# Kernel tuning notes

Hardware: AMD Instinct MI355X
Metric: run time of the kernel (lower is better)

## Reference

```python
import jax, jax.numpy as jnp
import numpy as np

EMB = 256
HID = 512
LAYERS = 4
VOCAB = 256
B = 16
T = 2048


def setup_inputs() -> dict:
    key = jax.random.key(0)
    ks = jax.random.split(key, 2 * LAYERS + 4)
    x = jax.random.randint(ks[0], (B, T), 0, VOCAB)
    emb = jax.random.uniform(ks[1], (VOCAB, EMB), minval=-0.1, maxval=0.1, dtype=jnp.float32)
    out = {"x": x, "emb": emb}
    for i in range(LAYERS):
        din = EMB if i == 0 else HID
        W = jax.random.normal(ks[2 + 2 * i], (din, 3 * HID), dtype=jnp.float32) * (1.0 / np.sqrt(din)).astype(np.float32)
        b = jnp.zeros((3 * HID,), jnp.float32)
        out[f"W{i}"] = W
        out[f"b{i}"] = b
    out["decW"] = jax.random.uniform(ks[2 + 2 * LAYERS], (HID, VOCAB), minval=-0.1, maxval=0.1, dtype=jnp.float32)
    out["decb"] = jnp.zeros((VOCAB,), jnp.float32)
    return out


def _fo_pool(z, f):
    # c_t = f_t * c_{t-1} + (1 - f_t) * z_t, c_{-1} = 0; z,f: (T, B, H)
    def step(c, zf):
        zt, ft = zf
        c = ft * c + (1.0 - ft) * zt
        return c, c
    c0 = jnp.zeros(z.shape[1:], z.dtype)
    _, C = jax.lax.scan(step, c0, (z, f))
    return C


def _qrnn_layer(x, W, b):
    # x: (T, B, D) time-major. One Linear producing Z,F,O gates, fo-pool, output gate.
    Y = jnp.einsum('tbd,dh->tbh', x, W) + b
    z, f, o = jnp.split(Y, 3, axis=-1)
    C = _fo_pool(jnp.tanh(z), jax.nn.sigmoid(f))
    return jax.nn.sigmoid(o) * C


def _dilated_layer(x, rate, W, b):
    # Fold time into batch by dilation rate, run QRNN, unfold (matches DRNN._prepare_inputs/_split_outputs)
    Tn, Bn, D = x.shape
    pad = (-Tn) % rate
    if pad:
        x = jnp.concatenate([x, jnp.zeros((pad, Bn, D), x.dtype)], axis=0)
    Tr = x.shape[0] // rate
    # dilated[t, j*B + b] = x[t*rate + j, b]
    xd = x.reshape(Tr, rate, Bn, D).reshape(Tr, rate * Bn, D)
    yd = _qrnn_layer(xd, W, b)  # (Tr, rate*B, H)
    Hd = yd.shape[-1]
    y = yd.reshape(Tr, rate, Bn, Hd).reshape(Tr * rate, Bn, Hd)[:Tn]
    return y


def reference(x, emb, W0, b0, W1, b1, W2, b2, W3, b3, decW, decb):
    h = emb[x]                    # (B, T, EMB) embedding lookup (dropout is identity at eval)
    h = h.transpose(1, 0, 2)      # time-major (T, B, EMB)
    Ws = [W0, W1, W2, W3]
    bs = [b0, b1, b2, b3]
    for i in range(LAYERS):
        h = _dilated_layer(h, 2 ** i, Ws[i], bs[i])
    h = h.transpose(1, 0, 2)      # (B, T, HID)
    return jnp.einsum('bth,hv->btv', h, decW) + decb
```

## Files before the change

### kernel.cpp

```cpp
#include <hip/hip_runtime.h>

#define TSEQ 2048
#define BATCH 16
#define EMBD 256
#define HID 512
#define NG 1536
#define NVOCAB 256
#define MROWS (TSEQ*BATCH)
#define CM 8192

typedef __attribute__((ext_vector_type(8))) unsigned short u16x8;
typedef __attribute__((ext_vector_type(8))) short s16x8;
typedef __attribute__((ext_vector_type(4))) float f32x4;

__device__ __forceinline__ float bf2f(unsigned short u) {
  union { unsigned u; float f; } x; x.u = ((unsigned)u) << 16; return x.f;
}
__device__ __forceinline__ unsigned short f2bf(float v) {
  union { float f; unsigned u; } x; x.f = v;
  unsigned r = (x.u + 0x7fffu + ((x.u >> 16) & 1u)) >> 16;
  return (unsigned short)r;
}
__device__ __forceinline__ float fast_rcp(float x) { return __builtin_amdgcn_rcpf(x); }
__device__ __forceinline__ float fast_sigmoid(float x) {
  float e = __builtin_amdgcn_exp2f(fminf(-1.442695041f * x, 80.f));
  return fast_rcp(1.f + e);
}
__device__ __forceinline__ float fast_tanh(float x) {
  float e = __builtin_amdgcn_exp2f(fminf(-2.885390082f * x, 80.f));
  return (1.f - e) * fast_rcp(1.f + e);
}
__device__ __forceinline__ void lds_cp16(const void* g, void* l) {
  __builtin_amdgcn_global_load_lds((const __attribute__((address_space(1))) void*)g,
                                   (__attribute__((address_space(3))) void*)l, 16, 0, 0);
}

__global__ __launch_bounds__(256) void embed_k(const int* __restrict__ x,
                                               const float* __restrict__ emb,
                                               unsigned short* __restrict__ H0) {
  int idx = blockIdx.x * 256 + threadIdx.x;
  int m = idx >> 5, e8 = (idx & 31) * 8;
  int tok = x[(m & 15) * TSEQ + (m >> 4)];
  const float* e = emb + (size_t)tok * EMBD + e8;
  float4 v0 = *(const float4*)e;
  float4 v1 = *(const float4*)(e + 4);
  u16x8 o;
  o[0]=f2bf(v0.x); o[1]=f2bf(v0.y); o[2]=f2bf(v0.z); o[3]=f2bf(v0.w);
  o[4]=f2bf(v1.x); o[5]=f2bf(v1.y); o[6]=f2bf(v1.z); o[7]=f2bf(v1.w);
  *(u16x8*)(H0 + (size_t)m * EMBD + e8) = o;
}

__global__ __launch_bounds__(256) void wt_k(const float* __restrict__ W,
                                            unsigned short* __restrict__ Wt,
                                            int K, int N) {
  __shared__ float tile[32][33];
  int n0 = blockIdx.x * 32, k0 = blockIdx.y * 32;
  int tx = threadIdx.x, ty = threadIdx.y;
#pragma unroll
  for (int i = 0; i < 4; ++i)
    tile[ty + i * 8][tx] = W[(size_t)(k0 + ty + i * 8) * N + n0 + tx];
  __syncthreads();
#pragma unroll
  for (int i = 0; i < 4; ++i)
    Wt[(size_t)(n0 + ty + i * 8) * K + k0 + tx] = f2bf(tile[tx][ty + i * 8]);
}

template <int K, int EPI>
__global__ __launch_bounds__(256) void gemm_k(const unsigned short* __restrict__ A,
                                              const unsigned short* __restrict__ Bt,
                                              const float* __restrict__ bias,
                                              unsigned short* __restrict__ Yg,
                                              float* __restrict__ Out) {
  __shared__ unsigned short smem[16384];
  unsigned short* sA = smem;
  unsigned short* sB = smem + 4096;
  const int tid = threadIdx.x;
  const int m0 = blockIdx.y * 128;
  const int n0 = blockIdx.x * 128;
  const int lane = tid & 63, wave = tid >> 6;
  const int wm = (wave >> 1) * 64, wn = (wave & 1) * 64;
  const int l15 = lane & 15, lg = lane >> 4;

  f32x4 acc[4][4] = {};

  for (int k0 = 0; k0 < K; k0 += 32) {
#pragma unroll
    for (int j = 0; j < 2; ++j) {
      int fl = j * 256 + tid;
      int m = fl >> 2;
      int cl = ((fl & 3) << 4) ^ (((m >> 1) & 3) << 4);
      lds_cp16(A + (size_t)(m0 + m) * K + k0 + (cl >> 1), &sA[fl * 8]);
      lds_cp16(Bt + (size_t)(n0 + m) * K + k0 + (cl >> 1), &sB[fl * 8]);
    }
    __syncthreads();

    s16x8 af[4], bf[4];
#pragma unroll
    for (int i = 0; i < 4; ++i) {
      int ma = wm + i * 16 + l15;
      int ca = (lg * 16) ^ (((ma >> 1) & 3) << 4);
      af[i] = *(const s16x8*)&sA[ma * 32 + (ca >> 1)];
      int nb = wn + i * 16 + l15;
      int cb = (lg * 16) ^ (((nb >> 1) & 3) << 4);
      bf[i] = *(const s16x8*)&sB[nb * 32 + (cb >> 1)];
    }
#pragma unroll
    for (int i = 0; i < 4; ++i)
#pragma unroll
      for (int j = 0; j < 4; ++j)
        acc[i][j] = __builtin_amdgcn_mfma_f32_16x16x32_bf16(af[i], bf[j], acc[i][j], 0, 0, 0);
    __syncthreads();
  }

  if (EPI == 0) {
    const int acttype = n0 >> 9;
#pragma unroll
    for (int i = 0; i < 4; ++i)
#pragma unroll
      for (int j = 0; j < 4; ++j)
#pragma unroll
        for (int r = 0; r < 4; ++r) {
          int mm = wm + i * 16 + lg * 4 + r;
          int nn = wn + j * 16 + l15;
          float v = acc[i][j][r] + bias[n0 + nn];
          v = (acttype == 0) ? fast_tanh(v) : fast_sigmoid(v);
          smem[mm * 128 + (nn ^ ((mm & 7) << 3))] = f2bf(v);
        }
    __syncthreads();
#pragma unroll
    for (int it = 0; it < 8; ++it) {
      int fl = it * 256 + tid;
      int mm = fl >> 4, ng = (fl & 15) * 8;
      u16x8 v = *(const u16x8*)&smem[mm * 128 + (ng ^ ((mm & 7) << 3))];
      *(u16x8*)(Yg + (size_t)(m0 + mm) * NG + n0 + ng) = v;
    }
  } else {
#pragma unroll
    for (int i = 0; i < 4; ++i)
#pragma unroll
      for (int j = 0; j < 4; ++j)
#pragma unroll
        for (int r = 0; r < 4; ++r) {
          int mmg = m0 + wm + i * 16 + lg * 4 + r;
          int nn = n0 + wn + j * 16 + l15;
          float v = acc[i][j][r] + bias[nn];
          int b = mmg & 15, t = mmg >> 4;
          Out[((size_t)b * TSEQ + t) * NVOCAB + nn] = v;
        }
  }
}

template <int LGS>
__global__ __launch_bounds__(256) void scan2_k(const unsigned short* __restrict__ Y,
                                               unsigned short* __restrict__ Hout,
                                               float* __restrict__ cst,
                                               int m0, int init) {
  const int S = 1 << LGS;
  const int HS = 1 << LGS;
  const int NSEG = 1 << (8 - LGS);
  __shared__ float As[256], Bs[256], Ci[256];

  const int tid = threadIdx.x;
  const int hi = tid & (HS - 1), seg = tid >> LGS;
  const int hg = blockIdx.x & ((2 * NSEG) - 1);
  const int s = blockIdx.x >> (9 - LGS);
  const int h = hg * HS + hi;
  const int mb = seg * 32 * S + s;

  float a = 1.f, c = 0.f;
#pragma unroll 8
  for (int t = 0; t < 32; ++t) {
    size_t ro = (size_t)(mb + t * S) * NG;
    float z = bf2f(Y[ro + h]);
    float f = bf2f(Y[ro + 512 + h]);
    a *= f;
    c = __builtin_fmaf(f, c - z, z);
  }
  As[seg * HS + hi] = a;
  Bs[seg * HS + hi] = c;
  __syncthreads();

  if (seg == 0) {
    float cc = init ? 0.f : cst[s * 512 + h];
#pragma unroll
    for (int k = 0; k < NSEG; ++k) {
      Ci[k * HS + hi] = cc;
      cc = __builtin_fmaf(As[k * HS + hi], cc, Bs[k * HS + hi]);
    }
    cst[s * 512 + h] = cc;
  }
  __syncthreads();

  c = Ci[seg * HS + hi];
#pragma unroll 8
  for (int t = 0; t < 32; ++t) {
    size_t ro = (size_t)(mb + t * S) * NG;
    float z = bf2f(Y[ro + h]);
    float f = bf2f(Y[ro + 512 + h]);
    float o = bf2f(Y[ro + 1024 + h]);
    c = __builtin_fmaf(f, c - z, z);
    Hout[(size_t)(m0 + mb + t * S) * HID + h] = f2bf(o * c);
  }
}

extern "C" void kernel_launch(void* const* d_in, const int* in_sizes, int n_in,
                              void* d_out, int out_size, void* d_ws, size_t ws_size,
                              hipStream_t stream) {
  const int* x = (const int*)d_in[0];
  const float* emb = (const float*)d_in[1];
  const float* Wl[4] = {(const float*)d_in[2], (const float*)d_in[4],
                        (const float*)d_in[6], (const float*)d_in[8]};
  const float* bl[4] = {(const float*)d_in[3], (const float*)d_in[5],
                        (const float*)d_in[7], (const float*)d_in[9]};
  const float* decW = (const float*)d_in[10];
  const float* decb = (const float*)d_in[11];
  float* out = (float*)d_out;

  if (ws_size < 64749568ull) return;
  char* ws = (char*)d_ws;
  unsigned short* Y   = (unsigned short*)(ws);
  unsigned short* Ha  = (unsigned short*)(ws + 25165824ull);
  unsigned short* Wt0 = (unsigned short*)(ws + 58720256ull);
  unsigned short* Wt1 = (unsigned short*)(ws + 59506688ull);
  unsigned short* Wt2 = (unsigned short*)(ws + 61079552ull);
  unsigned short* Wt3 = (unsigned short*)(ws + 62652416ull);
  unsigned short* WtD = (unsigned short*)(ws + 64225280ull);
  float*          cst = (float*)(ws + 64487424ull);
  unsigned short* Hb  = (unsigned short*)d_out;

  wt_k<<<dim3(NG / 32, EMBD / 32), dim3(32, 8), 0, stream>>>(Wl[0], Wt0, EMBD, NG);
  wt_k<<<dim3(NG / 32, HID / 32), dim3(32, 8), 0, stream>>>(Wl[1], Wt1, HID, NG);
  wt_k<<<dim3(NG / 32, HID / 32), dim3(32, 8), 0, stream>>>(Wl[2], Wt2, HID, NG);
  wt_k<<<dim3(NG / 32, HID / 32), dim3(32, 8), 0, stream>>>(Wl[3], Wt3, HID, NG);
  wt_k<<<dim3(NVOCAB / 32, HID / 32), dim3(32, 8), 0, stream>>>(decW, WtD, HID, NVOCAB);

  embed_k<<<(MROWS * (EMBD / 8)) / 256, 256, 0, stream>>>(x, emb, Ha);

  unsigned short* Wts[4] = {Wt0, Wt1, Wt2, Wt3};
  unsigned short* Hbuf[2] = {Ha, Hb};
  for (int L = 0; L < 4; ++L) {
    unsigned short* Hin = Hbuf[L & 1];
    unsigned short* Hout = Hbuf[(L + 1) & 1];
    const int Kd = (L == 0) ? EMBD : HID;
    for (int ch = 0; ch < MROWS / CM; ++ch) {
      const unsigned short* Ach = Hin + (size_t)ch * CM * Kd;
      if (L == 0)
        gemm_k<EMBD, 0><<<dim3(NG / 128, CM / 128), 256, 0, stream>>>(Ach, Wts[L], bl[L], Y, nullptr);
      else
        gemm_k<HID, 0><<<dim3(NG / 128, CM / 128), 256, 0, stream>>>(Ach, Wts[L], bl[L], Y, nullptr);
      switch (L) {
        case 0: scan2_k<4><<<512, 256, 0, stream>>>(Y, Hout, cst, ch * CM, ch == 0); break;
        case 1: scan2_k<5><<<512, 256, 0, stream>>>(Y, Hout, cst, ch * CM, ch == 0); break;
        case 2: scan2_k<6><<<512, 256, 0, stream>>>(Y, Hout, cst, ch * CM, ch == 0); break;
        case 3: scan2_k<7><<<512, 256, 0, stream>>>(Y, Hout, cst, ch * CM, ch == 0); break;
      }
    }
  }

  gemm_k<HID, 1><<<dim3(NVOCAB / 128, MROWS / 128), 256, 0, stream>>>(Hbuf[0], WtD, decb, nullptr, out);
}
```

Baseline: 709.1 us.

## Run each QRNN layer as one full-sequence GEMM plus one parallel scan

Drops the 4-chunk loop that split each layer into 8192-row GEMM and scan launches with carried state. Each layer now runs one GEMM over all rows into a larger Y buffer, followed by a scan kernel with a new block decomposition of 16 segments by 16 hidden units. That kernel launches more blocks for higher dilation rates. The change cuts launch count and removes the serial chunk dependency, but the Y workspace grows about fourfold and per-thread segments for low dilation become long (128 steps).

```diff
diff --git a/kernel.cpp b/kernel.cpp
--- a/kernel.cpp
+++ b/kernel.cpp
@@ -7,7 +7,6 @@
 #define NG 1536
 #define NVOCAB 256
 #define MROWS (TSEQ*BATCH)
-#define CM 8192
 
 typedef __attribute__((ext_vector_type(8))) unsigned short u16x8;
 typedef __attribute__((ext_vector_type(8))) short s16x8;
@@ -151,55 +150,57 @@
 }
 
 template <int LGS>
-__global__ __launch_bounds__(256) void scan2_k(const unsigned short* __restrict__ Y,
-                                               unsigned short* __restrict__ Hout,
-                                               float* __restrict__ cst,
-                                               int m0, int init) {
+__global__ __launch_bounds__(256) void scan3_k(const unsigned short* __restrict__ Y,
+                                               unsigned short* __restrict__ Hout) {
   const int S = 1 << LGS;
-  const int HS = 1 << LGS;
-  const int NSEG = 1 << (8 - LGS);
+  const int SEGLEN = 2048 >> LGS;
   __shared__ float As[256], Bs[256], Ci[256];
-
   const int tid = threadIdx.x;
-  const int hi = tid & (HS - 1), seg = tid >> LGS;
-  const int hg = blockIdx.x & ((2 * NSEG) - 1);
-  const int s = blockIdx.x >> (9 - LGS);
-  const int h = hg * HS + hi;
-  const int mb = seg * 32 * S + s;
+  const int hi = tid & 15, seg = tid >> 4;
+  const int s = blockIdx.x >> 5, hg = blockIdx.x & 31;
+  const int h = hg * 16 + hi;
+  const long rbase = (long)s + (long)seg * SEGLEN * S;
+  const size_t step = (size_t)S * NG;
 
   float a = 1.f, c = 0.f;
+  {
+    const unsigned short* p = Y + (size_t)rbase * NG + h;
 #pragma unroll 8
-  for (int t = 0; t < 32; ++t) {
-    size_t ro = (size_t)(mb + t * S) * NG;
-    float z = bf2f(Y[ro + h]);
-    float f = bf2f(Y[ro + 512 + h]);
-    a *= f;
+    for (int t = 0; t < SEGLEN; ++t) {
+      float z = bf2f(p[0]);
+      float f = bf2f(p[512]);
+      a *= f;
+      c = __builtin_fmaf(f, c - z, z);
+      p += step;
+    }
+  }
+  As[tid] = a;
+  Bs[tid] = c;
+  __syncthreads();
+
+  if (seg == 0) {
+    float cc = 0.f;
+#pragma unroll
+    for (int k = 0; k < 16; ++k) {
+      Ci[k * 16 + hi] = cc;
+      cc = __builtin_fmaf(As[k * 16 + hi], cc, Bs[k * 16 + hi]);
+    }
+  }
+  __syncthreads();
+
+  c = Ci[tid];
+  const unsigned short* p = Y + (size_t)rbase * NG + h;
+  unsigned short* hb = Hout + (size_t)rbase * HID + h;
+  const size_t stepH = (size_t)S * HID;
+#pragma unroll 4
+  for (int t = 0; t < SEGLEN; ++t) {
+    float z = bf2f(p[0]);
+    float f = bf2f(p[512]);
+    float o = bf2f(p[1024]);
     c = __builtin_fmaf(f, c - z, z);
-  }
-  As[seg * HS + hi] = a;
-  Bs[seg * HS + hi] = c;
-  __syncthreads();
-
-  if (seg == 0) {
-    float cc = init ? 0.f : cst[s * 512 + h];
-#pragma unroll
-    for (int k = 0; k < NSEG; ++k) {
-      Ci[k * HS + hi] = cc;
-      cc = __builtin_fmaf(As[k * HS + hi], cc, Bs[k * HS + hi]);
-    }
-    cst[s * 512 + h] = cc;
-  }
-  __syncthreads();
-
-  c = Ci[seg * HS + hi];
-#pragma unroll 8
-  for (int t = 0; t < 32; ++t) {
-    size_t ro = (size_t)(mb + t * S) * NG;
-    float z = bf2f(Y[ro + h]);
-    float f = bf2f(Y[ro + 512 + h]);
-    float o = bf2f(Y[ro + 1024 + h]);
-    c = __builtin_fmaf(f, c - z, z);
-    Hout[(size_t)(m0 + mb + t * S) * HID + h] = f2bf(o * c);
+    *hb = f2bf(o * c);
+    p += step;
+    hb += stepH;
   }
 }
 
@@ -216,16 +217,15 @@
   const float* decb = (const float*)d_in[11];
   float* out = (float*)d_out;
 
-  if (ws_size < 64749568ull) return;
+  if (ws_size < 139984896ull) return;
   char* ws = (char*)d_ws;
   unsigned short* Y   = (unsigned short*)(ws);
-  unsigned short* Ha  = (unsigned short*)(ws + 25165824ull);
-  unsigned short* Wt0 = (unsigned short*)(ws + 58720256ull);
-  unsigned short* Wt1 = (unsigned short*)(ws + 59506688ull);
-  unsigned short* Wt2 = (unsigned short*)(ws + 61079552ull);
-  unsigned short* Wt3 = (unsigned short*)(ws + 62652416ull);
-  unsigned short* WtD = (unsigned short*)(ws + 64225280ull);
-  float*          cst = (float*)(ws + 64487424ull);
+  unsigned short* Ha  = (unsigned short*)(ws + 100663296ull);
+  unsigned short* Wt0 = (unsigned short*)(ws + 134217728ull);
+  unsigned short* Wt1 = (unsigned short*)(ws + 135004160ull);
+  unsigned short* Wt2 = (unsigned short*)(ws + 136577024ull);
+  unsigned short* Wt3 = (unsigned short*)(ws + 138149888ull);
+  unsigned short* WtD = (unsigned short*)(ws + 139722752ull);
   unsigned short* Hb  = (unsigned short*)d_out;
 
   wt_k<<<dim3(NG / 32, EMBD / 32), dim3(32, 8), 0, stream>>>(Wl[0], Wt0, EMBD, NG);
@@ -236,26 +236,14 @@
 
   embed_k<<<(MROWS * (EMBD / 8)) / 256, 256, 0, stream>>>(x, emb, Ha);
 
-  unsigned short* Wts[4] = {Wt0, Wt1, Wt2, Wt3};
-  unsigned short* Hbuf[2] = {Ha, Hb};
-  for (int L = 0; L < 4; ++L) {
-    unsigned short* Hin = Hbuf[L & 1];
-    unsigned short* Hout = Hbuf[(L + 1) & 1];
-    const int Kd = (L == 0) ? EMBD : HID;
-    for (int ch = 0; ch < MROWS / CM; ++ch) {
-      const unsigned short* Ach = Hin + (size_t)ch * CM * Kd;
-      if (L == 0)
-        gemm_k<EMBD, 0><<<dim3(NG / 128, CM / 128), 256, 0, stream>>>(Ach, Wts[L], bl[L], Y, nullptr);
-      else
-        gemm_k<HID, 0><<<dim3(NG / 128, CM / 128), 256, 0, stream>>>(Ach, Wts[L], bl[L], Y, nullptr);
-      switch (L) {
-        case 0: scan2_k<4><<<512, 256, 0, stream>>>(Y, Hout, cst, ch * CM, ch == 0); break;
-        case 1: scan2_k<5><<<512, 256, 0, stream>>>(Y, Hout, cst, ch * CM, ch == 0); break;
-        case 2: scan2_k<6><<<512, 256, 0, stream>>>(Y, Hout, cst, ch * CM, ch == 0); break;
-        case 3: scan2_k<7><<<512, 256, 0, stream>>>(Y, Hout, cst, ch * CM, ch == 0); break;
-      }
-    }
-  }
-
-  gemm_k<HID, 1><<<dim3(NVOCAB / 128, MROWS / 128), 256, 0, stream>>>(Hbuf[0], WtD, decb, nullptr, out);
-}
+  gemm_k<EMBD, 0><<<dim3(NG / 128, MROWS / 128), 256, 0, stream>>>(Ha, Wt0, bl[0], Y, nullptr);
+  scan3_k<4><<<16 * 32, 256, 0, stream>>>(Y, Hb);
+  gemm_k<HID, 0><<<dim3(NG / 128, MROWS / 128), 256, 0, stream>>>(Hb, Wt1, bl[1], Y, nullptr);
+  scan3_k<5><<<32 * 32, 256, 0, stream>>>(Y, Ha);
+  gemm_k<HID, 0><<<dim3(NG / 128, MROWS / 128), 256, 0, stream>>>(Ha, Wt2, bl[2], Y, nullptr);
+  scan3_k<6><<<64 * 32, 256, 0, stream>>>(Y, Hb);
+  gemm_k<HID, 0><<<dim3(NG / 128, MROWS / 128), 256, 0, stream>>>(Hb, Wt3, bl[3], Y, nullptr);
+  scan3_k<7><<<128 * 32, 256, 0, stream>>>(Y, Ha);
+
+  gemm_k<HID, 1><<<dim3(NVOCAB / 128, MROWS / 128), 256, 0, stream>>>(Ha, WtD, decb, nullptr, out);
+}
```

Result: slower. 888.6 us (+25.3%).

## Remap scan kernel to 32-wide hidden groups with 8 time segments per block

Applied to the files above, without the earlier changes.

Reworks the chunked fo-pool scan so each block covers 32 contiguous hidden units and 8 time segments whose length depends on dilation, and scales the grid with the dilation rate instead of fixing it at 512 blocks. Each wavefront now reads 64 contiguous bytes per gate row rather than segment-dependent widths. Loads and stores use pointer increments in place of per-iteration index multiplies. In exchange, block count and segment length vary per layer, so layer 0 gets fewer blocks with longer serial segments while later layers get more blocks.

```diff
diff --git a/kernel.cpp b/kernel.cpp
--- a/kernel.cpp
+++ b/kernel.cpp
@@ -156,50 +156,56 @@
                                                float* __restrict__ cst,
                                                int m0, int init) {
   const int S = 1 << LGS;
-  const int HS = 1 << LGS;
-  const int NSEG = 1 << (8 - LGS);
+  const int SEGLEN = 1024 >> LGS;
   __shared__ float As[256], Bs[256], Ci[256];
 
   const int tid = threadIdx.x;
-  const int hi = tid & (HS - 1), seg = tid >> LGS;
-  const int hg = blockIdx.x & ((2 * NSEG) - 1);
-  const int s = blockIdx.x >> (9 - LGS);
-  const int h = hg * HS + hi;
-  const int mb = seg * 32 * S + s;
+  const int hi = tid & 31, seg = tid >> 5;
+  const int s = blockIdx.x >> 4, hg = blockIdx.x & 15;
+  const int h = hg * 32 + hi;
+  const int mb = seg * SEGLEN * S + s;
+  const size_t step = (size_t)S * NG;
 
   float a = 1.f, c = 0.f;
+  {
+    const unsigned short* p = Y + (size_t)mb * NG + h;
 #pragma unroll 8
-  for (int t = 0; t < 32; ++t) {
-    size_t ro = (size_t)(mb + t * S) * NG;
-    float z = bf2f(Y[ro + h]);
-    float f = bf2f(Y[ro + 512 + h]);
-    a *= f;
-    c = __builtin_fmaf(f, c - z, z);
-  }
-  As[seg * HS + hi] = a;
-  Bs[seg * HS + hi] = c;
+    for (int t = 0; t < SEGLEN; ++t) {
+      float z = bf2f(p[0]);
+      float f = bf2f(p[512]);
+      a *= f;
+      c = __builtin_fmaf(f, c - z, z);
+      p += step;
+    }
+  }
+  As[tid] = a;
+  Bs[tid] = c;
   __syncthreads();
 
   if (seg == 0) {
     float cc = init ? 0.f : cst[s * 512 + h];
 #pragma unroll
-    for (int k = 0; k < NSEG; ++k) {
-      Ci[k * HS + hi] = cc;
-      cc = __builtin_fmaf(As[k * HS + hi], cc, Bs[k * HS + hi]);
+    for (int k = 0; k < 8; ++k) {
+      Ci[k * 32 + hi] = cc;
+      cc = __builtin_fmaf(As[k * 32 + hi], cc, Bs[k * 32 + hi]);
     }
     cst[s * 512 + h] = cc;
   }
   __syncthreads();
 
-  c = Ci[seg * HS + hi];
-#pragma unroll 8
-  for (int t = 0; t < 32; ++t) {
-    size_t ro = (size_t)(mb + t * S) * NG;
-    float z = bf2f(Y[ro + h]);
-    float f = bf2f(Y[ro + 512 + h]);
-    float o = bf2f(Y[ro + 1024 + h]);
+  c = Ci[tid];
+  const unsigned short* p = Y + (size_t)mb * NG + h;
+  unsigned short* hb = Hout + (size_t)(m0 + mb) * HID + h;
+  const size_t stepH = (size_t)S * HID;
+#pragma unroll 4
+  for (int t = 0; t < SEGLEN; ++t) {
+    float z = bf2f(p[0]);
+    float f = bf2f(p[512]);
+    float o = bf2f(p[1024]);
     c = __builtin_fmaf(f, c - z, z);
-    Hout[(size_t)(m0 + mb + t * S) * HID + h] = f2bf(o * c);
+    *hb = f2bf(o * c);
+    p += step;
+    hb += stepH;
   }
 }
 
@@ -249,10 +255,10 @@
       else
         gemm_k<HID, 0><<<dim3(NG / 128, CM / 128), 256, 0, stream>>>(Ach, Wts[L], bl[L], Y, nullptr);
       switch (L) {
-        case 0: scan2_k<4><<<512, 256, 0, stream>>>(Y, Hout, cst, ch * CM, ch == 0); break;
-        case 1: scan2_k<5><<<512, 256, 0, stream>>>(Y, Hout, cst, ch * CM, ch == 0); break;
-        case 2: scan2_k<6><<<512, 256, 0, stream>>>(Y, Hout, cst, ch * CM, ch == 0); break;
-        case 3: scan2_k<7><<<512, 256, 0, stream>>>(Y, Hout, cst, ch * CM, ch == 0); break;
+        case 0: scan2_k<4><<<16 * 16, 256, 0, stream>>>(Y, Hout, cst, ch * CM, ch == 0); break;
+        case 1: scan2_k<5><<<32 * 16, 256, 0, stream>>>(Y, Hout, cst, ch * CM, ch == 0); break;
+        case 2: scan2_k<6><<<64 * 16, 256, 0, stream>>>(Y, Hout, cst, ch * CM, ch == 0); break;
+        case 3: scan2_k<7><<<128 * 16, 256, 0, stream>>>(Y, Hout, cst, ch * CM, ch == 0); break;
       }
     }
   }
```

Measured after the change: 701.4 us. About the same (-1.1%).
